# Kernel tuning notes

Hardware: AMD Instinct MI355X
Metric: run time of the kernel (lower is better)

Reference implementation:

```python
import jax, jax.numpy as jnp
import numpy as np

VOCAB, TAGS, EDIM, HDIM = 50000, 32, 256, 512
HALF = HDIM // 2
NEG = -10000.0


def _lstm_dir(x, Wih, Whh, b, reverse):
    # x: [B,S,E]; Wih: [4H,E]; Whh: [4H,H]; b: [4H] (b_ih + b_hh fused).
    B = x.shape[0]
    H = Whh.shape[1]

    def cell(carry, xt):
        h, c = carry
        z = xt @ Wih.T + h @ Whh.T + b            # [B,4H], gate order i,f,g,o
        i, f, g, o = jnp.split(z, 4, axis=-1)
        c = jax.nn.sigmoid(f) * c + jax.nn.sigmoid(i) * jnp.tanh(g)
        h = jax.nn.sigmoid(o) * jnp.tanh(c)
        return (h, c), h

    h0 = jnp.zeros((B, H), x.dtype)
    xs = jnp.swapaxes(x, 0, 1)                    # [S,B,E]
    _, hs = jax.lax.scan(cell, (h0, h0), xs, reverse=reverse)
    return jnp.swapaxes(hs, 0, 1)                 # [B,S,H] aligned to input positions


def _viterbi(feats, trans):
    # feats: [B,S,T] emissions; trans[prev, next] as used in the original recursion.
    B, S, T = feats.shape
    v0 = jnp.full((B, T), NEG, feats.dtype).at[:, 0].set(0.0)

    def step(v, feat_t):
        scores = v[:, :, None] + trans[None]      # [B, prev, next]
        best = jnp.max(scores, axis=1)
        bp = jnp.argmax(scores, axis=1)           # [B,T]
        return best + feat_t, bp

    vT, bps = jax.lax.scan(step, v0, jnp.swapaxes(feats, 0, 1))   # bps: [S,B,T]
    term = vT + trans[0][None]                    # terminal uses transitions[0, :]
    best_scores = jnp.max(term, axis=1)           # [B]
    last_tag = jnp.argmax(term, axis=1)           # [B]

    bidx = jnp.arange(B)

    def back(tag, bp):
        return bp[bidx, tag], tag

    tag0, ys = jax.lax.scan(back, last_tag, bps[1:], reverse=True)  # ys[k] = tag at pos k+1
    paths = jnp.concatenate([tag0[:, None], jnp.swapaxes(ys, 0, 1)], axis=1)  # [B,S]
    return paths, best_scores


def setup_inputs() -> dict:
    key = jax.random.key(0)
    ks = jax.random.split(key, 12)
    B, S = 64, 256
    s = 0.05
    trans = jax.random.normal(ks[10], (TAGS, TAGS), jnp.float32)
    trans = trans.at[:, 0].set(NEG).at[0, :].set(NEG)
    return {
        "sentence": jax.random.randint(ks[0], (B, S), 0, VOCAB, jnp.int32),
        "embed": jax.random.normal(ks[1], (VOCAB, EDIM), jnp.float32) * s,
        "Wih_f": jax.random.normal(ks[2], (4 * HALF, EDIM), jnp.float32) * s,
        "Whh_f": jax.random.normal(ks[3], (4 * HALF, HALF), jnp.float32) * s,
        "b_f": jax.random.normal(ks[4], (4 * HALF,), jnp.float32) * s,
        "Wih_b": jax.random.normal(ks[5], (4 * HALF, EDIM), jnp.float32) * s,
        "Whh_b": jax.random.normal(ks[6], (4 * HALF, HALF), jnp.float32) * s,
        "b_b": jax.random.normal(ks[7], (4 * HALF,), jnp.float32) * s,
        "Wout": jax.random.normal(ks[8], (TAGS, HDIM), jnp.float32) * s,
        "bout": jax.random.normal(ks[9], (TAGS,), jnp.float32) * s,
        "trans": trans,
    }


def reference(sentence, embed, Wih_f, Whh_f, b_f, Wih_b, Whh_b, b_b, Wout, bout, trans):
    # Inference path: dropout is identity in eval mode.
    x = embed[sentence]                           # [B,S,E]
    h_f = _lstm_dir(x, Wih_f, Whh_f, b_f, reverse=False)
    h_b = _lstm_dir(x, Wih_b, Whh_b, b_b, reverse=True)
    h = jnp.concatenate([h_f, h_b], axis=-1)      # [B,S,HDIM]
    feats = h @ Wout.T + bout                     # [B,S,TAGS]
    paths, scores = _viterbi(feats, trans)
    return paths, scores
```

## Files before the change

kernel.cpp:

```cpp
#include <hip/hip_runtime.h>
#include <hip/hip_fp16.h>
#include <stdint.h>

typedef float  f32x4  __attribute__((ext_vector_type(4)));
typedef int    i32x4  __attribute__((ext_vector_type(4)));
typedef short  bf16x8 __attribute__((ext_vector_type(8)));
typedef _Float16 h2v  __attribute__((ext_vector_type(2)));

#define NEGV -10000.0f
#define LOG2E 1.442695041f

__device__ __forceinline__ unsigned short f32_to_bf16(float f){
  union { float f; uint32_t u; } v; v.f = f;
  uint32_t u = v.u;
  u += 0x7fffu + ((u >> 16) & 1u);
  return (unsigned short)(u >> 16);
}
__device__ __forceinline__ float bf16_lo(uint32_t u){
  union { uint32_t u; float f; } v; v.u = (u & 0xffffu) << 16; return v.f;
}
__device__ __forceinline__ float bf16_hi(uint32_t u){
  union { uint32_t u; float f; } v; v.u = u & 0xffff0000u; return v.f;
}
__device__ __forceinline__ float fsig(float x){
  return __builtin_amdgcn_rcpf(1.0f + __builtin_exp2f(-LOG2E * x));
}
__device__ __forceinline__ float ftanh_(float x){
  return 1.0f - 2.0f * __builtin_amdgcn_rcpf(1.0f + __builtin_exp2f(2.0f * LOG2E * x));
}
__device__ __forceinline__ uint32_t enc_i8(float x){
  int v = (int)rintf(x * 512.0f);
  v = v > 127 ? 127 : (v < -127 ? -127 : v);
  return (uint32_t)(v & 0xff);
}
__device__ __forceinline__ float fdot2f(uint32_t w, uint32_t h, float acc){
#if __has_builtin(__builtin_amdgcn_fdot2)
  union { uint32_t u; h2v h; } a, b;
  a.u = w; b.u = h;
  return __builtin_amdgcn_fdot2(a.h, b.h, acc, false);
#else
  acc += __half2float(__ushort_as_half((unsigned short)(w & 0xffffu))) *
         __half2float(__ushort_as_half((unsigned short)(h & 0xffffu)));
  acc += __half2float(__ushort_as_half((unsigned short)(w >> 16))) *
         __half2float(__ushort_as_half((unsigned short)(h >> 16)));
  return acc;
#endif
}
__device__ __forceinline__ void wg_barrier_lds(){
  __builtin_amdgcn_s_waitcnt(0xC07F);
  asm volatile("" ::: "memory");
  __builtin_amdgcn_s_barrier();
  asm volatile("" ::: "memory");
}
__device__ __forceinline__ void wave_lds_fence(){
  __builtin_amdgcn_s_waitcnt(0xC07F);
  asm volatile("" ::: "memory");
}
__device__ __forceinline__ float vpack(float sc, int p){
  const int i = (__float_as_int(sc) & 0xFFFFFFE0) | p;
  return __int_as_float(i);
}

__global__ __launch_bounds__(256) void k_quant(
    const float* __restrict__ whh_f, const float* __restrict__ whh_b,
    uint32_t* __restrict__ wq)
{
  const int id  = blockIdx.x * 256 + threadIdx.x;
  const int dir = id >> 16;
  const int rem = id & 0xffff;
  const int np  = rem >> 6;
  const int d   = rem & 63;
  const int u = np >> 2, g = np & 3;
  const float* __restrict__ w = dir ? whh_b : whh_f;
  const float4 v = *(const float4*)(w + (size_t)(g * 256 + u) * 256 + d * 4);
  wq[id] = enc_i8(v.x) | (enc_i8(v.y) << 8) | (enc_i8(v.z) << 16) | (enc_i8(v.w) << 24);
}

__global__ __launch_bounds__(256) void k_xproj(
    const int* __restrict__ sent, const float* __restrict__ embed,
    const float* __restrict__ wih_f, const float* __restrict__ wih_b,
    const float* __restrict__ bias_f, const float* __restrict__ bias_b,
    unsigned short* __restrict__ xp)
{
  __shared__ __align__(16) short At[128 * 32];
  __shared__ __align__(16) short Bt[128 * 32];
  const int bid = blockIdx.x;
  const int tm = bid >> 4;
  const int tn = bid & 15;
  const int dir = tn >> 3;
  const int nloc0 = (tn & 7) * 128;
  const float* __restrict__ wsrc = dir ? wih_b : wih_f;
  const float* __restrict__ bsrc = dir ? bias_b : bias_f;

  const int tid = threadIdx.x;
  const int wv = tid >> 6;
  const int lane = tid & 63;
  const int lr = lane & 15;
  const int lq = lane >> 4;

  const int r  = tid >> 1;
  const int ch = (tid & 1) * 16;

  const int tok = sent[tm * 128 + r];
  const int nprow = nloc0 + r;
  const float* arow = embed + (size_t)tok * 256 + ch;
  const float* brow = wsrc + (size_t)((nprow & 3) * 256 + (nprow >> 2)) * 256 + ch;
  short* at_dst = At + r * 32 + ch;
  short* bt_dst = Bt + r * 32 + ch;

  f32x4 acc[2][8];
  #pragma unroll
  for (int i = 0; i < 2; i++)
    #pragma unroll
    for (int n = 0; n < 8; n++)
      acc[i][n] = (f32x4){0.f, 0.f, 0.f, 0.f};

  for (int k0 = 0; k0 < 256; k0 += 32) {
    #pragma unroll
    for (int qq = 0; qq < 4; qq++) {
      const float4 va = *(const float4*)(arow + k0 + qq * 4);
      const float4 vb = *(const float4*)(brow + k0 + qq * 4);
      short4 sa, sb;
      sa.x = (short)f32_to_bf16(va.x); sa.y = (short)f32_to_bf16(va.y);
      sa.z = (short)f32_to_bf16(va.z); sa.w = (short)f32_to_bf16(va.w);
      sb.x = (short)f32_to_bf16(vb.x); sb.y = (short)f32_to_bf16(vb.y);
      sb.z = (short)f32_to_bf16(vb.z); sb.w = (short)f32_to_bf16(vb.w);
      *(short4*)(at_dst + qq * 4) = sa;
      *(short4*)(bt_dst + qq * 4) = sb;
    }
    __syncthreads();
    bf16x8 bfr[8];
    #pragma unroll
    for (int n = 0; n < 8; n++)
      bfr[n] = *(const bf16x8*)(Bt + (n * 16 + lr) * 32 + lq * 8);
    #pragma unroll
    for (int i = 0; i < 2; i++) {
      const bf16x8 af = *(const bf16x8*)(At + (wv * 32 + i * 16 + lr) * 32 + lq * 8);
      #pragma unroll
      for (int n = 0; n < 8; n++)
        acc[i][n] = __builtin_amdgcn_mfma_f32_16x16x32_bf16(af, bfr[n], acc[i][n], 0, 0, 0);
    }
    __syncthreads();
  }
  #pragma unroll
  for (int i = 0; i < 2; i++) {
    #pragma unroll
    for (int n = 0; n < 8; n++) {
      const int nloc = nloc0 + n * 16 + lr;
      const float bias = bsrc[(nloc & 3) * 256 + (nloc >> 2)];
      #pragma unroll
      for (int rr = 0; rr < 4; rr++) {
        const int m = tm * 128 + wv * 32 + i * 16 + lq * 4 + rr;
        xp[(size_t)m * 2048 + dir * 1024 + nloc] = f32_to_bf16(acc[i][n][rr] + bias);
      }
    }
  }
}

__global__ __launch_bounds__(512, 2) void k_lstm(
    const unsigned short* __restrict__ xp, const uint32_t* __restrict__ wq,
    __half* __restrict__ hout)
{
  __shared__ __align__(16) unsigned char hbuf[2][256];
  const int bid = blockIdx.x;
  const int dir = bid & 1;
  const int b = bid >> 1;
  const int tid = threadIdx.x;
  const int w = tid >> 6;
  const int l = tid & 63;
  const int lr = l & 15;
  const int q = l >> 4;
  const int nio = lr & 7;
  const int u = w * 32 + nio * 4 + q;

  i32x4 afr[8][4];
  {
    const unsigned char* wb = (const unsigned char*)wq + (size_t)dir * 262144;
    #pragma unroll
    for (int ni = 0; ni < 8; ni++) {
      const unsigned char* rp = wb + (size_t)(w * 128 + ni * 16 + lr) * 256 + q * 16;
      #pragma unroll
      for (int kt = 0; kt < 4; kt++) {
        afr[ni][kt] = *(const i32x4*)(rp + kt * 64);
        asm volatile("" : "+v"(afr[ni][kt].x), "+v"(afr[ni][kt].y),
                          "+v"(afr[ni][kt].z), "+v"(afr[ni][kt].w));
      }
    }
  }
  if (tid < 64) ((uint32_t*)hbuf[0])[tid] = 0;
  float c = 0.0f;
  const unsigned short* xpo = xp + (size_t)b * (256 * 2048) + dir * 1024
                                 + w * 128 + nio * 16 + q * 4;
  __half* hb = hout + (size_t)b * (256 * 512) + dir * 256 + u;

  uint2 xa, xb;
  {
    const int t0 = dir ? 255 : 0;
    const int t1 = dir ? 254 : 1;
    xa = *(const uint2*)(xpo + (size_t)t0 * 2048);
    xb = *(const uint2*)(xpo + (size_t)t1 * 2048);
  }
  __syncthreads();

#define LSTM_STEP(SS, SRD, SWR, XC)                                          \
  {                                                                          \
    const int t_ = dir ? (255 - (SS)) : (SS);                                \
    i32x4 bfr[4];                                                            \
    _Pragma("unroll")                                                        \
    for (int kt = 0; kt < 4; kt++)                                           \
      bfr[kt] = *(const i32x4*)(&hbuf[SRD][kt * 64 + q * 16]);               \
    i32x4 acc[8];                                                            \
    _Pragma("unroll")                                                        \
    for (int ni = 0; ni < 8; ni++) acc[ni] = (i32x4){0, 0, 0, 0};            \
    _Pragma("unroll")                                                        \
    for (int kt = 0; kt < 4; kt++)                                           \
      _Pragma("unroll")                                                      \
      for (int ni = 0; ni < 8; ni++)                                         \
        acc[ni] = __builtin_amdgcn_mfma_i32_16x16x64_i8(                     \
            afr[ni][kt], bfr[kt], acc[ni], 0, 0, 0);                         \
    i32x4 zi = acc[0];                                                       \
    _Pragma("unroll")                                                        \
    for (int ni = 1; ni < 8; ni++) {                                         \
      const bool own = (nio == ni);                                          \
      zi.x = own ? acc[ni].x : zi.x;                                         \
      zi.y = own ? acc[ni].y : zi.y;                                         \
      zi.z = own ? acc[ni].z : zi.z;                                         \
      zi.w = own ? acc[ni].w : zi.w;                                         \
    }                                                                        \
    const float SINV = 1.0f / 65536.0f;                                      \
    const float z_i = (float)zi.x * SINV + bf16_lo(XC.x);                    \
    const float z_f = (float)zi.y * SINV + bf16_hi(XC.x);                    \
    const float z_g = (float)zi.z * SINV + bf16_lo(XC.y);                    \
    const float z_o = (float)zi.w * SINV + bf16_hi(XC.y);                    \
    const float ig = fsig(z_i), fg = fsig(z_f);                              \
    const float gg = ftanh_(z_g), og = fsig(z_o);                            \
    c = fg * c + ig * gg;                                                    \
    const float h_ = og * ftanh_(c);                                         \
    {                                   \
      int spf = (SS) + 2; spf = spf > 255 ? 255 : spf;                       \
      const int tpf = dir ? (255 - spf) : spf;                               \
      XC = *(const uint2*)(xpo + (size_t)tpf * 2048);                        \
    }                                                                        \
    if (lr < 8) {                                                            \
      hb[(size_t)t_ * 512] = __float2half(h_);                               \
      int hq = (int)rintf(h_ * 128.0f);                                      \
      hq = hq > 127 ? 127 : (hq < -127 ? -127 : hq);                         \
      hbuf[SWR][u] = (unsigned char)(hq & 0xff);                             \
    }                                                                        \
    wg_barrier_lds();                                                        \
  }

  for (int s = 0; s < 256; s += 2) {
    LSTM_STEP(s,     0, 1, xa)
    LSTM_STEP(s + 1, 1, 0, xb)
  }
#undef LSTM_STEP
}

__global__ __launch_bounds__(256) void k_feats(
    const __half* __restrict__ hg, const float* __restrict__ wout,
    const float* __restrict__ bout, float* __restrict__ feats)
{
  __shared__ uint32_t W2[32 * 257];
  __shared__ float bo[32];
  const int b  = blockIdx.x >> 2;
  const int t0 = (blockIdx.x & 3) * 64;
  const int tid = threadIdx.x;
  #pragma unroll
  for (int i = 0; i < 32; i++) {
    const float2 v = *(const float2*)(wout + (size_t)i * 512 + tid * 2);
    const uint32_t lo = (uint32_t)__half_as_ushort(__float2half(v.x));
    const uint32_t hi = (uint32_t)__half_as_ushort(__float2half(v.y));
    W2[i * 257 + tid] = lo | (hi << 16);
  }
  if (tid < 32) bo[tid] = bout[tid];
  __syncthreads();
  const int n = tid & 31;
  const int tg = tid >> 5;
  const uint32_t* hrow0 = (const uint32_t*)(hg + (size_t)b * (256 * 512));
  for (int tt = 0; tt < 8; tt++) {
    const int t = t0 + tg * 8 + tt;
    const uint4* hr = (const uint4*)(hrow0 + t * 256);
    float a0 = 0.f, a1 = 0.f, a2 = 0.f, a3 = 0.f;
    #pragma unroll
    for (int qd = 0; qd < 64; qd++) {
      const uint4 hq = hr[qd];
      a0 = fdot2f(W2[n * 257 + qd * 4 + 0], hq.x, a0);
      a1 = fdot2f(W2[n * 257 + qd * 4 + 1], hq.y, a1);
      a2 = fdot2f(W2[n * 257 + qd * 4 + 2], hq.z, a2);
      a3 = fdot2f(W2[n * 257 + qd * 4 + 3], hq.w, a3);
    }
    feats[((size_t)b * 256 + t) * 32 + n] = bo[n] + ((a0 + a1) + (a2 + a3));
  }
}

__global__ __launch_bounds__(64) void k_viterbi(
    const float* __restrict__ feats, const float* __restrict__ trans,
    int* __restrict__ paths, float* __restrict__ scores)
{
  __shared__ float vbuf[2][2][32];
  __shared__ unsigned char bp[2][256][32];
  __shared__ int tags[2][256];
  const int tid = threadIdx.x;
  const int s = tid >> 5;
  const int n = tid & 31;
  const int b = blockIdx.x * 2 + s;
  float tcol[32];
  #pragma unroll
  for (int p = 0; p < 32; p++) tcol[p] = trans[p * 32 + n];
  float v = (n == 0) ? -20000.0f : (NEGV - 20000.0f);
  const float* fb = feats + (size_t)b * (256 * 32) + n;
  float xf0 = fb[0], xf1 = fb[32], xf2 = fb[64], xf3 = fb[96];

  for (int t = 0; t < 256; t++) {
    const int ph = t & 1;
    vbuf[ph][s][n] = v;
    wave_lds_fence();
    float g0, g1, g2, g3, g4, g5, g6, g7;
    #define VGROUP(GI, DST)                                                   \
    {                                                                         \
      const float4 q4 = ((const float4*)vbuf[ph][s])[GI];                     \
      const float p0 = vpack(q4.x + tcol[GI * 4 + 0], GI * 4 + 0);            \
      const float p1 = vpack(q4.y + tcol[GI * 4 + 1], GI * 4 + 1);            \
      const float p2 = vpack(q4.z + tcol[GI * 4 + 2], GI * 4 + 2);            \
      const float p3 = vpack(q4.w + tcol[GI * 4 + 3], GI * 4 + 3);            \
      DST = fmaxf(fmaxf(p0, p1), fmaxf(p2, p3));                              \
    }
    VGROUP(0, g0) VGROUP(1, g1) VGROUP(2, g2) VGROUP(3, g3)
    VGROUP(4, g4) VGROUP(5, g5) VGROUP(6, g6) VGROUP(7, g7)
    #undef VGROUP
    const float best = fmaxf(fmaxf(fmaxf(g0, g1), fmaxf(g2, g3)),
                             fmaxf(fmaxf(g4, g5), fmaxf(g6, g7)));
    bp[s][t][n] = (unsigned char)(__float_as_int(best) & 31);
    v = best + xf0;
    xf0 = xf1; xf1 = xf2; xf2 = xf3;
    {
      int tp = t + 4; tp = tp > 255 ? 255 : tp;
      xf3 = fb[(size_t)tp * 32];
    }
  }
  vbuf[0][s][n] = v + tcol[0];
  wave_lds_fence();
  if (n == 0) {
    float bs = vbuf[0][s][0]; int bt = 0;
    #pragma unroll 1
    for (int p = 1; p < 32; p++) {
      if (vbuf[0][s][p] > bs) { bs = vbuf[0][s][p]; bt = p; }
    }
    scores[b] = bs + 20000.0f;
    int tg = bt;
    tags[s][255] = tg;
    #pragma unroll 1
    for (int t = 255; t >= 1; t--) {
      tg = bp[s][t][tg];
      tags[s][t - 1] = tg;
    }
  }
  wave_lds_fence();
  #pragma unroll
  for (int i = 0; i < 8; i++) {
    const int idx = i * 64 + tid;
    const int ss = idx >> 8;
    const int t = idx & 255;
    paths[(size_t)(blockIdx.x * 2 + ss) * 256 + t] = tags[ss][t];
  }
}

extern "C" void kernel_launch(void* const* d_in, const int* in_sizes, int n_in,
                              void* d_out, int out_size, void* d_ws, size_t ws_size,
                              hipStream_t stream)
{
  (void)in_sizes; (void)n_in; (void)out_size; (void)ws_size;
  const int*   sent  = (const int*)d_in[0];
  const float* embed = (const float*)d_in[1];
  const float* wih_f = (const float*)d_in[2];
  const float* whh_f = (const float*)d_in[3];
  const float* b_f   = (const float*)d_in[4];
  const float* wih_b = (const float*)d_in[5];
  const float* whh_b = (const float*)d_in[6];
  const float* b_b   = (const float*)d_in[7];
  const float* wout  = (const float*)d_in[8];
  const float* bout  = (const float*)d_in[9];
  const float* trans = (const float*)d_in[10];

  char* ws = (char*)d_ws;
  unsigned short* XP = (unsigned short*)(ws);
  __half*   Hg = (__half*)(ws + 67108864);
  uint32_t* WQ = (uint32_t*)(ws + 83886080);
  float*    FT = (float*)(ws + 84410368);

  int*   paths  = (int*)d_out;
  float* scores = (float*)d_out + 16384;

  k_quant  <<<dim3(512),  dim3(256), 0, stream>>>(whh_f, whh_b, WQ);
  k_xproj  <<<dim3(2048), dim3(256), 0, stream>>>(sent, embed, wih_f, wih_b, b_f, b_b, XP);
  k_lstm   <<<dim3(128),  dim3(512), 0, stream>>>(XP, WQ, Hg);
  k_feats  <<<dim3(256),  dim3(256), 0, stream>>>(Hg, wout, bout, FT);
  k_viterbi<<<dim3(32),   dim3(64),  0, stream>>>(FT, trans, paths, scores);
}
```

Before: 541.9 us.

## Split Viterbi max across half-waves, restructure feats loop, seed MFMA with zero

The Viterbi kernel now runs one sequence per block, with each half-wave covering 16 predecessor tags and the two halves combined by a cross-lane shuffle. This shortens the serial per-step max chain and doubles the block count. The feats kernel is reorganized to hold a chunk of weights in registers as 128-bit LDS loads and reuse it across 8 timesteps, at the cost of more register use. The LSTM step initializes its accumulators from the first MFMA against a zero constant instead of explicit zeroing, and adds a clobber of four high VGPRs, which may perturb register allocation.

New measurement: 507.2 us. 1.07x faster.

```diff
diff --git a/kernel.cpp b/kernel.cpp
--- a/kernel.cpp
+++ b/kernel.cpp
@@ -173,6 +173,8 @@
   const int nio = lr & 7;
   const int u = w * 32 + nio * 4 + q;
 
+  asm volatile("" ::: "v200", "v201", "v202", "v203");
+
   i32x4 afr[8][4];
   {
     const unsigned char* wb = (const unsigned char*)wq + (size_t)dir * 262144;
@@ -189,6 +191,7 @@
   }
   if (tid < 64) ((uint32_t*)hbuf[0])[tid] = 0;
   float c = 0.0f;
+  const i32x4 kz = (i32x4){0, 0, 0, 0};
   const unsigned short* xpo = xp + (size_t)b * (256 * 2048) + dir * 1024
                                  + w * 128 + nio * 16 + q * 4;
   __half* hb = hout + (size_t)b * (256 * 512) + dir * 256 + u;
@@ -211,9 +214,11 @@
       bfr[kt] = *(const i32x4*)(&hbuf[SRD][kt * 64 + q * 16]);               \
     i32x4 acc[8];                                                            \
     _Pragma("unroll")                                                        \
-    for (int ni = 0; ni < 8; ni++) acc[ni] = (i32x4){0, 0, 0, 0};            \
+    for (int ni = 0; ni < 8; ni++)                                           \
+      acc[ni] = __builtin_amdgcn_mfma_i32_16x16x64_i8(                       \
+          afr[ni][0], bfr[0], kz, 0, 0, 0);                                  \
     _Pragma("unroll")                                                        \
-    for (int kt = 0; kt < 4; kt++)                                           \
+    for (int kt = 1; kt < 4; kt++)                                           \
       _Pragma("unroll")                                                      \
       for (int ni = 0; ni < 8; ni++)                                         \
         acc[ni] = __builtin_amdgcn_mfma_i32_16x16x64_i8(                     \
@@ -261,7 +266,7 @@
     const __half* __restrict__ hg, const float* __restrict__ wout,
     const float* __restrict__ bout, float* __restrict__ feats)
 {
-  __shared__ uint32_t W2[32 * 257];
+  __shared__ __align__(16) uint32_t W2[32 * 260];
   __shared__ float bo[32];
   const int b  = blockIdx.x >> 2;
   const int t0 = (blockIdx.x & 3) * 64;
@@ -271,26 +276,41 @@
     const float2 v = *(const float2*)(wout + (size_t)i * 512 + tid * 2);
     const uint32_t lo = (uint32_t)__half_as_ushort(__float2half(v.x));
     const uint32_t hi = (uint32_t)__half_as_ushort(__float2half(v.y));
-    W2[i * 257 + tid] = lo | (hi << 16);
+    W2[i * 260 + tid] = lo | (hi << 16);
   }
   if (tid < 32) bo[tid] = bout[tid];
   __syncthreads();
   const int n = tid & 31;
   const int tg = tid >> 5;
   const uint32_t* hrow0 = (const uint32_t*)(hg + (size_t)b * (256 * 512));
+  float a[8];
+  #pragma unroll
+  for (int tt = 0; tt < 8; tt++) a[tt] = 0.0f;
+  for (int ck = 0; ck < 8; ck++) {
+    uint4 wch[8];
+    #pragma unroll
+    for (int j = 0; j < 8; j++)
+      wch[j] = *(const uint4*)(&W2[n * 260 + ck * 32 + j * 4]);
+    #pragma unroll
+    for (int tt = 0; tt < 8; tt++) {
+      const int t = t0 + tg * 8 + tt;
+      const uint4* hr = (const uint4*)(hrow0 + t * 256 + ck * 32);
+      float acc = a[tt];
+      #pragma unroll
+      for (int j = 0; j < 8; j++) {
+        const uint4 hq = hr[j];
+        acc = fdot2f(wch[j].x, hq.x, acc);
+        acc = fdot2f(wch[j].y, hq.y, acc);
+        acc = fdot2f(wch[j].z, hq.z, acc);
+        acc = fdot2f(wch[j].w, hq.w, acc);
+      }
+      a[tt] = acc;
+    }
+  }
+  #pragma unroll
   for (int tt = 0; tt < 8; tt++) {
     const int t = t0 + tg * 8 + tt;
-    const uint4* hr = (const uint4*)(hrow0 + t * 256);
-    float a0 = 0.f, a1 = 0.f, a2 = 0.f, a3 = 0.f;
-    #pragma unroll
-    for (int qd = 0; qd < 64; qd++) {
-      const uint4 hq = hr[qd];
-      a0 = fdot2f(W2[n * 257 + qd * 4 + 0], hq.x, a0);
-      a1 = fdot2f(W2[n * 257 + qd * 4 + 1], hq.y, a1);
-      a2 = fdot2f(W2[n * 257 + qd * 4 + 2], hq.z, a2);
-      a3 = fdot2f(W2[n * 257 + qd * 4 + 3], hq.w, a3);
-    }
-    feats[((size_t)b * 256 + t) * 32 + n] = bo[n] + ((a0 + a1) + (a2 + a3));
+    feats[((size_t)b * 256 + t) * 32 + n] = bo[n] + a[tt];
   }
 }
 
@@ -298,40 +318,40 @@
     const float* __restrict__ feats, const float* __restrict__ trans,
     int* __restrict__ paths, float* __restrict__ scores)
 {
-  __shared__ float vbuf[2][2][32];
-  __shared__ unsigned char bp[2][256][32];
-  __shared__ int tags[2][256];
+  __shared__ __align__(16) float vbuf[32];
+  __shared__ unsigned char bp[256][32];
+  __shared__ int tags[256];
   const int tid = threadIdx.x;
-  const int s = tid >> 5;
   const int n = tid & 31;
-  const int b = blockIdx.x * 2 + s;
-  float tcol[32];
-  #pragma unroll
-  for (int p = 0; p < 32; p++) tcol[p] = trans[p * 32 + n];
+  const int hf = tid >> 5;
+  const int b = blockIdx.x;
+  float tcol[16];
+  #pragma unroll
+  for (int p = 0; p < 16; p++) tcol[p] = trans[(hf * 16 + p) * 32 + n];
   float v = (n == 0) ? -20000.0f : (NEGV - 20000.0f);
   const float* fb = feats + (size_t)b * (256 * 32) + n;
   float xf0 = fb[0], xf1 = fb[32], xf2 = fb[64], xf3 = fb[96];
 
   for (int t = 0; t < 256; t++) {
-    const int ph = t & 1;
-    vbuf[ph][s][n] = v;
+    if (hf == 0) vbuf[n] = v;
     wave_lds_fence();
-    float g0, g1, g2, g3, g4, g5, g6, g7;
-    #define VGROUP(GI, DST)                                                   \
+    float g0, g1, g2, g3;
+    #define VG(GI, DST)                                                       \
     {                                                                         \
-      const float4 q4 = ((const float4*)vbuf[ph][s])[GI];                     \
-      const float p0 = vpack(q4.x + tcol[GI * 4 + 0], GI * 4 + 0);            \
-      const float p1 = vpack(q4.y + tcol[GI * 4 + 1], GI * 4 + 1);            \
-      const float p2 = vpack(q4.z + tcol[GI * 4 + 2], GI * 4 + 2);            \
-      const float p3 = vpack(q4.w + tcol[GI * 4 + 3], GI * 4 + 3);            \
-      DST = fmaxf(fmaxf(p0, p1), fmaxf(p2, p3));                              \
-    }
-    VGROUP(0, g0) VGROUP(1, g1) VGROUP(2, g2) VGROUP(3, g3)
-    VGROUP(4, g4) VGROUP(5, g5) VGROUP(6, g6) VGROUP(7, g7)
-    #undef VGROUP
-    const float best = fmaxf(fmaxf(fmaxf(g0, g1), fmaxf(g2, g3)),
-                             fmaxf(fmaxf(g4, g5), fmaxf(g6, g7)));
-    bp[s][t][n] = (unsigned char)(__float_as_int(best) & 31);
+      const float4 q4 = ((const float4*)vbuf)[hf * 4 + GI];                   \
+      const int p0 = hf * 16 + GI * 4;                                        \
+      const float c0 = vpack(q4.x + tcol[GI * 4 + 0], p0 + 0);                \
+      const float c1 = vpack(q4.y + tcol[GI * 4 + 1], p0 + 1);                \
+      const float c2 = vpack(q4.z + tcol[GI * 4 + 2], p0 + 2);                \
+      const float c3 = vpack(q4.w + tcol[GI * 4 + 3], p0 + 3);                \
+      DST = fmaxf(fmaxf(c0, c1), fmaxf(c2, c3));                              \
+    }
+    VG(0, g0) VG(1, g1) VG(2, g2) VG(3, g3)
+    #undef VG
+    const float hbest = fmaxf(fmaxf(g0, g1), fmaxf(g2, g3));
+    const float other = __shfl_xor(hbest, 32, 64);
+    const float best = fmaxf(hbest, other);
+    if (hf == 0) bp[t][n] = (unsigned char)(__float_as_int(best) & 31);
     v = best + xf0;
     xf0 = xf1; xf1 = xf2; xf2 = xf3;
     {
@@ -339,30 +359,28 @@
       xf3 = fb[(size_t)tp * 32];
     }
   }
-  vbuf[0][s][n] = v + tcol[0];
+  if (hf == 0) vbuf[n] = v + tcol[0];
   wave_lds_fence();
-  if (n == 0) {
-    float bs = vbuf[0][s][0]; int bt = 0;
+  if (tid == 0) {
+    float bs = vbuf[0]; int bt = 0;
     #pragma unroll 1
     for (int p = 1; p < 32; p++) {
-      if (vbuf[0][s][p] > bs) { bs = vbuf[0][s][p]; bt = p; }
+      if (vbuf[p] > bs) { bs = vbuf[p]; bt = p; }
     }
     scores[b] = bs + 20000.0f;
     int tg = bt;
-    tags[s][255] = tg;
+    tags[255] = tg;
     #pragma unroll 1
     for (int t = 255; t >= 1; t--) {
-      tg = bp[s][t][tg];
-      tags[s][t - 1] = tg;
+      tg = bp[t][tg];
+      tags[t - 1] = tg;
     }
   }
   wave_lds_fence();
   #pragma unroll
-  for (int i = 0; i < 8; i++) {
-    const int idx = i * 64 + tid;
-    const int ss = idx >> 8;
-    const int t = idx & 255;
-    paths[(size_t)(blockIdx.x * 2 + ss) * 256 + t] = tags[ss][t];
+  for (int i = 0; i < 4; i++) {
+    const int t = i * 64 + tid;
+    paths[(size_t)b * 256 + t] = tags[t];
   }
 }
 
@@ -396,5 +414,5 @@
   k_xproj  <<<dim3(2048), dim3(256), 0, stream>>>(sent, embed, wih_f, wih_b, b_f, b_b, XP);
   k_lstm   <<<dim3(128),  dim3(512), 0, stream>>>(XP, WQ, Hg);
   k_feats  <<<dim3(256),  dim3(256), 0, stream>>>(Hg, wout, bout, FT);
-  k_viterbi<<<dim3(32),   dim3(64),  0, stream>>>(FT, trans, paths, scores);
-}
+  k_viterbi<<<dim3(64),   dim3(64),  0, stream>>>(FT, trans, paths, scores);
+}
```
